# Optimization experiments

Measured on AMD Instinct MI355X. Metric: run time of the kernel, lower is better.

Reference implementation:

```python
import jax, jax.numpy as jnp
import numpy as np
from jax.scipy.special import logsumexp, gammaln

B, F, T = 4, 256, 256
K, L, C, D, N = 8, 1, 10, 156, 2
A00, A10 = 0.99, 0.99
NEG = -1.0e9


def setup_inputs():
    ks = jax.random.split(jax.random.key(0), 12)
    def p(i, shape, s=0.05):
        return jax.random.normal(ks[i], shape, jnp.float32) * s
    A = jnp.array([[A00, 1.0 - A00], [A10, 1.0 - A10]], jnp.float32)
    return dict(
        h=jax.random.normal(ks[0], (B, F, T), jnp.float32),
        logit_lo1=jax.random.normal(ks[1], (K, C, 1), jnp.float32),
        log_A=jnp.broadcast_to(jnp.log(A), (K, C, N, N)),
        dur_conc=p(2, (K, C, N, L), 1.0),
        dur_rate=p(3, (K, C, N, L), 1.0),
        dur_mix=p(4, (K, C, N, L), 1.0),
        w_mix=p(5, (F, F)), b_mix=jnp.zeros((F,), jnp.float32),
        q_attn=p(6, (F,)), w_attn=p(7, (F, F)), b_attn=jnp.zeros((F,), jnp.float32),
        w_k=p(8, (K, F)), b_k=jnp.zeros((K,), jnp.float32),
        bn_gamma=jnp.ones((F,), jnp.float32), bn_beta=jnp.zeros((F,), jnp.float32),
        w_em=p(9, (C * N * K, F)), b_em=jnp.zeros((C * N * K,), jnp.float32),
    )


def gamma_duration(conc_raw, rate_raw, mix_raw):
    # L-component gamma mixture over durations 1..D, normalized over D. [K,C,N,D]
    a = jax.nn.softplus(conc_raw) + 1e-4
    b = jax.nn.softplus(rate_raw) + 1e-4
    d = jnp.arange(1, D + 1, dtype=jnp.float32)
    logpdf = (a[..., None] * jnp.log(b)[..., None] - gammaln(a)[..., None]
              + (a[..., None] - 1.0) * jnp.log(d) - b[..., None] * d)  # [K,C,N,L,D]
    logw = jax.nn.log_softmax(mix_raw, axis=-1)
    lp = logsumexp(logw[..., None] + logpdf, axis=-2)  # [K,C,N,D]
    return jax.nn.log_softmax(lp, axis=-1)


def emission(h, bn_gamma, bn_beta, w_em, b_em):
    # BatchNorm1d (training-mode batch stats) -> ReLU -> 1x1 Conv -> rearrange
    mean = h.mean(axis=(0, 2), keepdims=True)
    var = ((h - mean) ** 2).mean(axis=(0, 2), keepdims=True)
    x = (h - mean) / jnp.sqrt(var + 1e-5) * bn_gamma[None, :, None] + bn_beta[None, :, None]
    x = jax.nn.relu(x)
    y = jnp.einsum('of,bft->bot', w_em, x) + b_em[None, :, None]  # [B, K*C*N, T]
    return y.reshape(B, K, C, N, T)


def mixture_ratio(h, w_mix, b_mix, q_attn, w_attn, b_attn, w_k, b_k):
    # 1x1 Conv -> ReLU -> attention pooling over T -> Linear(F,K) -> log_softmax
    x = jax.nn.relu(jnp.einsum('of,bft->bot', w_mix, h) + b_mix[None, :, None])  # [B,F,T]
    scores = jnp.einsum('f,bft->bt', q_attn, x)
    w = jax.nn.softmax(scores, axis=-1)
    pooled = jnp.einsum('bft,bt->bf', x, w)
    z = pooled @ w_attn.T + b_attn
    logits = z @ w_k.T + b_k
    return jax.nn.log_softmax(logits, axis=-1)  # [B,K]


def compute_log_b(logp_x):
    # log_b[...,d,t] = sum_{i=0}^{d} logp_x[...,t-i] (d<=t), else -10.  [B,K,C,N,D,T]
    src = jnp.arange(T)[None, :] - jnp.arange(D)[:, None]  # [D,T]
    valid = src >= 0
    g = logp_x[:, :, :, :, jnp.clip(src, 0, T - 1)]        # [B,K,C,N,D,T]
    g = jnp.where(valid, g, 0.0)
    lb = jnp.cumsum(g, axis=-2)
    return jnp.where(valid, lb, -10.0)


def hsmm_forward(logp_x, log_lo, logp_d, log_A):
    log_b = compute_log_b(logp_x)                          # [B,K,C,N,D,T]
    log_c = logp_d[None, :, :, :, :, None] + log_b
    darange = jnp.arange(D)
    dclip = jnp.minimum(jnp.arange(T), D - 1)
    lb_diag = log_b[:, :, :, :, dclip, jnp.arange(T)]      # [B,K,C,N,T]
    xs = (jnp.arange(T),
          jnp.moveaxis(log_c, -1, 0),                      # [T,B,K,C,N,D]
          jnp.moveaxis(lb_diag, -1, 0),                    # [T,B,K,C,N]
          jnp.moveaxis(logp_d[:, :, :, dclip], -1, 0))     # [T,K,C,N]
    S0 = jnp.full((B, K, C, N, D), NEG)                    # S[...,j] = s[t-1-j]

    def step(S, x):
        t, logc_t, lbd_t, pd_t = x
        # trans[...,m,j] = lse_n(S[...,n,j] + log_A[n,m])
        trans = logsumexp(S[:, :, :, :, None, :] + log_A[None, :, :, :, :, None], axis=3)
        init_t = log_lo[None] + pd_t[None] + lbd_t         # [B,K,C,N]
        alpha_t = jnp.where(darange == t, init_t[..., None],
                            jnp.where(darange < t, trans + logc_t, NEG))
        s_t = logsumexp(alpha_t, axis=-1)
        S_new = jnp.concatenate([s_t[..., None], S[..., :-1]], axis=-1)
        return S_new, alpha_t

    _, alphas = jax.lax.scan(step, S0, xs)
    return jnp.moveaxis(alphas, 0, -1), log_b              # [B,K,C,N,D,T]


def hsmm_backward(log_b, logp_d, log_A):
    j_idx = jnp.arange(D - 1)
    tau = jnp.arange(T)[None, :] + 1 + j_idx[:, None]      # [D-1,T]
    valid = tau <= T - 1
    # M[...,j,t] = log_b[...,j,t+1+j]
    M = log_b[:, :, :, :, j_idx[:, None], jnp.clip(tau, 0, T - 1)]
    M = jnp.where(valid, M, NEG)
    xs_M = jnp.moveaxis(M[..., :T - 1], -1, 0)             # [T-1,B,K,C,N,D-1]
    pd = logp_d[..., :D - 1]                               # [K,C,N,D-1]
    buf0 = jnp.full((B, K, C, N, D - 1), NEG).at[..., 0].set(0.0)

    def step(buf, M_t):
        val = M_t + buf + pd[None]                         # [B,K,C,m,j]
        tot = log_A[None, :, :, :, :, None] + val[:, :, :, None, :, :]  # [B,K,C,n,m,j]
        beta_t = logsumexp(tot, axis=(4, 5))               # [B,K,C,N]
        buf_new = jnp.concatenate([beta_t[..., None], buf[..., :-1]], axis=-1)
        return buf_new, beta_t

    _, betas = jax.lax.scan(step, buf0, xs_M, reverse=True)
    return jnp.concatenate([jnp.moveaxis(betas, 0, -1),
                            jnp.zeros((B, K, C, N, 1))], axis=-1)  # [B,K,C,N,T]


def calc_logp_event(log_alpha, log_beta, log_pi):
    log_gamma = log_alpha + log_beta[..., None, :]
    Z = logsumexp(log_alpha[..., -1], axis=(-2, -1))       # [B,K,C]
    lp = log_gamma - Z[..., None, None, None]
    return logsumexp(log_pi[:, :, None, None, None, None] + lp, axis=1)  # [B,C,N,D,T]


def calc_p_frame(logp_event):
    d_idx = jnp.arange(D)[:, None]
    s_idx = jnp.arange(T)[None, :]

    def per_t(t):
        mask = (s_idx >= d_idx) & (s_idx >= t) & (s_idx <= t + d_idx)  # [D,T]
        lp = jnp.where(mask[None, None, None], logp_event, NEG)
        return logsumexp(lp, axis=(-2, -1))                # [B,C,N]

    lj = jax.lax.map(per_t, jnp.arange(T))                 # [T,B,C,N]
    pj = jax.nn.softmax(jnp.moveaxis(lj, 0, -1), axis=2)   # [B,C,N,T]
    return pj[:, :, 1]


def reference(h, logit_lo1, log_A, dur_conc, dur_rate, dur_mix, w_mix, b_mix,
              q_attn, w_attn, b_attn, w_k, b_k, bn_gamma, bn_beta, w_em, b_em):
    logp_x = emission(h, bn_gamma, bn_beta, w_em, b_em)    # [B,K,C,N,T]
    log_pi = mixture_ratio(h, w_mix, b_mix, q_attn, w_attn, b_attn, w_k, b_k)
    log_lo = jax.nn.log_sigmoid(jnp.stack([logit_lo1, -logit_lo1], axis=2))[..., 0]  # [K,C,N]
    logp_d = gamma_duration(dur_conc, dur_rate, dur_mix)   # [K,C,N,D]
    log_alpha, log_b = hsmm_forward(logp_x, log_lo, logp_d, log_A)
    log_beta = hsmm_backward(log_b, logp_d, log_A)
    logp_event = calc_logp_event(log_alpha, log_beta, log_pi)
    p_frame = calc_p_frame(logp_event)
    return logp_event, p_frame
```

## Files before the change

### kernel.cpp

```cpp
#include <hip/hip_runtime.h>
#include <math.h>

#define BB_ 4
#define FF_ 256
#define TT_ 256
#define KK_ 8
#define CC_ 10
#define DD_ 156
#define OO_ 160
#define NEGC (-1e9f)

__device__ __forceinline__ float softplusf(float x){
    return fmaxf(x, 0.f) + log1pf(expf(-fabsf(x)));
}
__device__ __forceinline__ float lse2f(float a, float b){
    float m = fmaxf(a, b);
    return m + logf(expf(a-m) + expf(b-m));
}
__device__ __forceinline__ float lse2_fast(float a, float b){
    float m = fmaxf(a, b);
    return m + __logf(__expf(a-m) + __expf(b-m));
}
__device__ __forceinline__ void lse_acc(float &m, float &s, float x){
    if (x > m){ s = s*expf(m-x) + 1.f; m = x; }
    else        s += expf(x-m);
}
__device__ __forceinline__ void lse_acc_fast(float &m, float &s, float x){
    if (x > m){ s = s*__expf(m-x) + 1.f; m = x; }
    else        s += __expf(x-m);
}
__device__ __forceinline__ void wave_lse_reduce(float &m, float &s){
    for (int off = 32; off; off >>= 1){
        float m2 = __shfl_xor(m, off);
        float s2 = __shfl_xor(s, off);
        float M  = fmaxf(m, m2);
        s = s*expf(m-M) + s2*expf(m2-M);
        m = M;
    }
}
template<int CTRL>
__device__ __forceinline__ float dppf(float v){
    return __int_as_float(__builtin_amdgcn_update_dpp(
        0, __float_as_int(v), CTRL, 0xF, 0xF, false));
}
__device__ __forceinline__ float dpp_sum8(float a){
    a = a + dppf<0x122>(a);
    a = a + dppf<0x124>(a);
    a = a + dppf<0x128>(a);
    return a;
}
__device__ __forceinline__ float dpp_max8(float a){
    a = fmaxf(a, dppf<0x122>(a));
    a = fmaxf(a, dppf<0x124>(a));
    a = fmaxf(a, dppf<0x128>(a));
    return a;
}

__global__ void k_bnstats_logpd(const float* __restrict__ h, float* __restrict__ meanv,
                                float* __restrict__ rstdv,
                                const float* __restrict__ conc, const float* __restrict__ rate,
                                const float* __restrict__ logit_lo1, float* __restrict__ logp_d,
                                float* __restrict__ log_lo){
    if (blockIdx.x >= FF_){
        if (threadIdx.x >= 64) return;
        int kcn = blockIdx.x - FF_;
        int lane = threadIdx.x;
        float a  = softplusf(conc[kcn]) + 1e-4f;
        float bb = softplusf(rate[kcn]) + 1e-4f;
        float base = a*logf(bb) - lgammaf(a);
        float vals[3]; int ds[3]; int cnt = 0;
        float m = -1e30f, s = 0.f;
        for (int i = 0; i < 3; ++i){
            int d = lane + i*64;
            if (d < DD_){
                float dv = (float)(d+1);
                float x = base + (a - 1.f)*logf(dv) - bb*dv;
                vals[cnt] = x; ds[cnt] = d; ++cnt;
                lse_acc(m, s, x);
            }
        }
        wave_lse_reduce(m, s);
        float total = m + logf(s);
        for (int i = 0; i < cnt; ++i) logp_d[kcn*DD_ + ds[i]] = vals[i] - total;
        if (lane == 0){
            float x = logit_lo1[kcn >> 1];
            float xx = (kcn & 1) ? -x : x;
            log_lo[kcn] = -softplusf(-xx);
        }
        return;
    }
    int f = blockIdx.x; int tid = threadIdx.x;
    float s = 0.f, s2 = 0.f;
    for (int b = 0; b < BB_; ++b){
        float v = h[(b*FF_ + f)*TT_ + tid];
        s += v; s2 += v*v;
    }
    __shared__ float rs[4], rs2[4];
    for (int off = 32; off; off >>= 1){ s += __shfl_xor(s, off); s2 += __shfl_xor(s2, off); }
    if ((tid & 63) == 0){ rs[tid>>6] = s; rs2[tid>>6] = s2; }
    __syncthreads();
    if (tid == 0){
        float S = rs[0]+rs[1]+rs[2]+rs[3];
        float S2 = rs2[0]+rs2[1]+rs2[2]+rs2[3];
        float mean = S / 1024.f;
        float var = S2 / 1024.f - mean*mean;
        meanv[f] = mean;
        rstdv[f] = rsqrtf(var + 1e-5f);
    }
}

__global__ void k_bnapply(const float* __restrict__ h, const float* __restrict__ meanv,
                          const float* __restrict__ rstdv, const float* __restrict__ gamma,
                          const float* __restrict__ beta, float* __restrict__ xbn){
    int idx = blockIdx.x*256 + threadIdx.x;
    int f = (idx >> 8) & 255;
    float x = (h[idx] - meanv[f]) * rstdv[f] * gamma[f] + beta[f];
    xbn[idx] = fmaxf(x, 0.f);
}

__global__ void k_gemm_em(const float* __restrict__ xbn, const float* __restrict__ w_em,
                          const float* __restrict__ b_em, float* __restrict__ Pout){
    int bid = blockIdx.x;
    int b = bid / OO_, o = bid % OO_;
    int t = threadIdx.x;
    const float* xb = xbn + b*FF_*TT_ + t;
    const float* wr = w_em + o*FF_;
    float acc = b_em[o];
    #pragma unroll 8
    for (int f = 0; f < FF_; ++f) acc += wr[f] * xb[f*TT_];
    __shared__ float buf[256];
    buf[t] = acc; __syncthreads();
    for (int off = 1; off < 256; off <<= 1){
        float x = (t >= off) ? buf[t-off] : 0.f;
        __syncthreads();
        buf[t] += x;
        __syncthreads();
    }
    Pout[bid*TT_ + t] = buf[t];
}

__global__ void k_attnpool(const float* __restrict__ xm, const float* __restrict__ xmT,
                           const float* __restrict__ q,
                           const float* __restrict__ w_attn, const float* __restrict__ b_attn,
                           const float* __restrict__ w_k, const float* __restrict__ b_k,
                           float* __restrict__ log_pi){
    int b = blockIdx.x; int tid = threadIdx.x;
    __shared__ float sc[256], pooled[256], zs[256], red[8];
    const float* xb = xm + b*FF_*TT_;
    float acc = 0.f;
    for (int f = 0; f < FF_; ++f) acc += q[f] * xb[f*TT_ + tid];
    sc[tid] = acc; __syncthreads();
    float v = sc[tid];
    float m = v;
    for (int off = 32; off; off >>= 1) m = fmaxf(m, __shfl_xor(m, off));
    if ((tid & 63) == 0) red[tid>>6] = m;
    __syncthreads();
    m = fmaxf(fmaxf(red[0], red[1]), fmaxf(red[2], red[3]));
    float e = expf(v - m);
    float ssum = e;
    for (int off = 32; off; off >>= 1) ssum += __shfl_xor(ssum, off);
    if ((tid & 63) == 0) red[4 + (tid>>6)] = ssum;
    __syncthreads();
    ssum = red[4]+red[5]+red[6]+red[7];
    __syncthreads();
    sc[tid] = e / ssum; __syncthreads();
    const float* xT = xmT + b*TT_*FF_;
    float pacc = 0.f;
    for (int t2 = 0; t2 < TT_; ++t2) pacc += xT[t2*FF_ + tid] * sc[t2];
    pooled[tid] = pacc; __syncthreads();
    int wv = tid >> 6; int ln = tid & 63;
    for (int ii = 0; ii < 64; ++ii){
        int i = wv*64 + ii;
        float za = 0.f;
        #pragma unroll
        for (int ff = 0; ff < 4; ++ff) za += pooled[ln + 64*ff] * w_attn[i*FF_ + ln + 64*ff];
        for (int off = 32; off; off >>= 1) za += __shfl_xor(za, off);
        if (ln == 0) zs[i] = za + b_attn[i];
    }
    __syncthreads();
    if (wv == 0){
        for (int kk2 = 0; kk2 < KK_; ++kk2){
            float za = 0.f;
            #pragma unroll
            for (int ff = 0; ff < 4; ++ff) za += zs[ln + 64*ff] * w_k[kk2*FF_ + ln + 64*ff];
            for (int off = 32; off; off >>= 1) za += __shfl_xor(za, off);
            if (ln == 0) red[kk2] = za + b_k[kk2];
        }
    }
    __syncthreads();
    if (tid == 0){
        float mm = -1e30f;
        for (int i = 0; i < KK_; ++i) mm = fmaxf(mm, red[i]);
        float su = 0.f;
        for (int i = 0; i < KK_; ++i) su += expf(red[i] - mm);
        sc[0] = mm + logf(su);
    }
    __syncthreads();
    if (tid < KK_) log_pi[b*KK_ + tid] = red[tid] - sc[0];
}

__global__ __launch_bounds__(256) void k_scan_mix(const float* __restrict__ P,
                          const float* __restrict__ logp_d,
                          const float* __restrict__ log_lo, const float* __restrict__ log_A,
                          float* __restrict__ s_hist, float* __restrict__ Zout,
                          float* __restrict__ beta,
                          const float* __restrict__ h, const float* __restrict__ w_mix,
                          const float* __restrict__ b_mix, float* __restrict__ xm,
                          float* __restrict__ xmT){
    __shared__ float L[11056];
    if (blockIdx.x >= 2*BB_*KK_*CC_/4){
        int bid = blockIdx.x - 2*BB_*KK_*CC_/4;
        int b = bid >> 8, o = bid & 255;
        int t = threadIdx.x;
        const float* hb = h + b*FF_*TT_ + t;
        const float* wr = w_mix + o*FF_;
        float acc = b_mix[o];
        #pragma unroll 8
        for (int f = 0; f < FF_; ++f) acc += wr[f] * hb[f*TT_];
        float v = fmaxf(acc, 0.f);
        xm[bid*TT_ + t] = v;
        xmT[(b*TT_ + t)*FF_ + o] = v;
        return;
    }
    if (threadIdx.x >= 64) return;
    int sbid = blockIdx.x;
    float* hist = L;
    float* pdL  = L + 8*424;
    float* EL   = pdL + 8*168;
    float* PL   = EL + 8*204;
    float* oL   = PL + 8*257;
    float* fsL  = oL + 8*257;
    float* ctL  = fsL + 8*36;
    int lane = threadIdx.x;
    int ch = lane >> 4, r = lane & 15, n = r & 1, q = r >> 1;
    int g = ch*2 + n, go = g ^ 1;
    bool fwd = sbid < (BB_*KK_*CC_/4);
    int gid0 = (fwd ? sbid : sbid - BB_*KK_*CC_/4) * 4;
    int dlim = fwd ? DD_ : (DD_-1);
    for (int idx = lane; idx < 8*168; idx += 64){
        int g2 = idx/168, d2 = idx%168;
        int gg = gid0 + (g2>>1); int c3 = gg % CC_, k3 = (gg/CC_) % KK_;
        pdL[g2*168 + d2] = (d2 < dlim) ? logp_d[((k3*CC_+c3)*2+(g2&1))*DD_ + d2] : -1e30f;
    }
    for (int idx = lane; idx < 4*512; idx += 64){
        int c2 = idx >> 9, j = idx & 511;
        PL[(c2*2 + (j>>8))*257 + (j&255)] = P[(size_t)(gid0+c2)*512 + j];
    }
    int gidc = gid0 + ch; int c = gidc % CC_, k = (gidc/CC_) % KK_;
    const float* Akc = log_A + (k*CC_+c)*4;
    float Epdn[4], Epdf[16];
    #pragma unroll
    for (int i = 0; i < 4; ++i)  Epdn[i] = __expf(pdL[g*168 + q + 8*i]);
    #pragma unroll
    for (int i = 0; i < 16; ++i) Epdf[i] = __expf(pdL[g*168 + 32 + q + 8*i]);

    if (fwd){
        for (int idx = lane; idx < 8*160; idx += 64)
            hist[(idx/160)*424 + (idx%160)] = -1e30f;
        float Aself = Akc[3*n], Across = Akc[2-n];
        float EAs = __expf(Aself);
        float EAc = __expf(Across);
        float llo = log_lo[(k*CC_+c)*2 + n];
        float Etp, pre[4];
        for (int t0 = 0; t0 < TT_; t0 += 32){
            asm volatile("" ::: "memory");
            float v[20];
            #pragma unroll
            for (int i = 0; i < 20; ++i) v[i] = hist[g*424 + t0 + q + 8*i];
            float z[10];
            #pragma unroll
            for (int i = 0; i < 10; ++i) z[i] = fmaxf(v[2*i], v[2*i+1]);
            #pragma unroll
            for (int i = 0; i < 5; ++i) z[i] = fmaxf(z[2*i], z[2*i+1]);
            float mt = fmaxf(fmaxf(fmaxf(z[0],z[1]), fmaxf(z[2],z[3])), z[4]);
            mt = dpp_max8(mt);
            float pm = -1e30f;
            #pragma unroll
            for (int j = 0; j < 4; ++j){
                int t = t0 + q + 8*j;
                pm = fmaxf(pm, (t < 168) ? pdL[g*168 + t] : -1e30f);
            }
            pm = dpp_max8(pm);
            mt = fmaxf(mt, llo + pm);
            #pragma unroll
            for (int i = 0; i < 20; ++i) EL[g*204 + q + 8*i] = __expf(v[i] - mt);
            float mto = dppf<0xB1>(mt);
            #pragma unroll
            for (int j = 0; j < 4; ++j){
                int tt = q + 8*j; int t = t0 + tt;
                float dP = PL[go*257 + t] - PL[g*257 + t];
                ctL[g*36 + tt] = fminf(EAc * __expf(dP + mto - mt), 1e15f);
            }
            asm volatile("" ::: "memory");
            for (int tt = 0; tt < 32; ++tt){
                float a0 = 0.f, a1 = 0.f;
                #pragma unroll
                for (int i = 0; i < 16; i += 2){
                    a0 = fmaf(EL[g*204 + 127 + tt - q - 8*i],     Epdf[i],   a0);
                    a1 = fmaf(EL[g*204 + 127 + tt - q - 8*(i+1)], Epdf[i+1], a1);
                }
                float a = dpp_sum8(a0 + a1);
                int t = t0 + tt;
                float pdt = (t < 168) ? pdL[g*168 + t] : -1e30f;
                if (r < 2) fsL[g*36 + tt] = a + __expf(llo + pdt - mt);
            }
            asm volatile("" ::: "memory");
            Etp = EL[g*204 + 159];
            #pragma unroll
            for (int i = 0; i < 4; ++i) pre[i] = EL[g*204 + 159 - q - 8*i];
            for (int tt = 0; tt < 32; ++tt){
                int t = t0 + tt;
                float x0 = ((q == 0) ? Etp : pre[0]) * Epdn[0];
                float ac = fmaf(pre[1], Epdn[1], x0);
                ac = fmaf(pre[2], Epdn[2], ac);
                ac = fmaf(pre[3], Epdn[3], ac);
                #pragma unroll
                for (int i = 0; i < 4; ++i) pre[i] = EL[g*204 + 160 + tt - q - 8*i];
                float S = dpp_sum8(ac) + fsL[g*36 + tt];
                S = fminf(fmaxf(S, 1e-30f), 1e15f);
                float So = dppf<0xB1>(S);
                float Et = fminf(fmaf(So, ctL[g*36 + tt], S*EAs), 1e30f);
                float lS = __logf(S), lE = __logf(Et);
                if (r < 2){
                    EL[g*204 + 160 + tt] = Et;
                    hist[g*424 + 160 + t] = lE + mt;
                    oL[g*257 + t] = lS + mt + PL[g*257 + t];
                }
                Etp = Et;
            }
        }
        asm volatile("" ::: "memory");
        for (int idx = lane; idx < 4*512; idx += 64){
            int c2 = idx >> 9, j = idx & 511;
            s_hist[(size_t)(gid0+c2)*512 + j] = oL[(c2*2 + (j>>8))*257 + (j&255)];
        }
        if (r == 0) Zout[gidc] = lse2f(oL[(ch*2)*257 + 255], oL[(ch*2+1)*257 + 255]);
    } else {
        for (int idx = lane; idx < 8*168; idx += 64)
            hist[(idx/168)*424 + 256 + (idx%168)] = -1e30f;
        if (lane < 8){
            hist[lane*424 + 255] = PL[lane*257 + 255];
            oL[lane*257 + 255] = 0.f;
        }
        float Aown = Akc[3*n], Aoth = Akc[n+1];
        float EAo = __expf(Aown);
        float EAx = __expf(Aoth);
        float Ewp, pre[4];
        for (int t0 = TT_-32; t0 >= 0; t0 -= 32){
            asm volatile("" ::: "memory");
            float v[20];
            #pragma unroll
            for (int i = 0; i < 20; ++i) v[i] = hist[g*424 + t0 + 32 + q + 8*i];
            float z[10];
            #pragma unroll
            for (int i = 0; i < 10; ++i) z[i] = fmaxf(v[2*i], v[2*i+1]);
            #pragma unroll
            for (int i = 0; i < 5; ++i) z[i] = fmaxf(z[2*i], z[2*i+1]);
            float mw = fmaxf(fmaxf(fmaxf(z[0],z[1]), fmaxf(z[2],z[3])), z[4]);
            mw = dpp_max8(mw);
            mw = fmaxf(mw, PL[g*257 + 255]);
            #pragma unroll
            for (int i = 0; i < 20; ++i) EL[g*204 + 32 + q + 8*i] = __expf(v[i] - mw);
            float mwo = dppf<0xB1>(mw);
            #pragma unroll
            for (int j = 0; j < 4; ++j){
                int tt = q + 8*j; int t = t0 + tt;
                float dP = PL[g*257 + t] - PL[go*257 + t];
                ctL[g*36 + tt] = fminf(EAx * __expf(dP + mwo - mw), 1e15f);
            }
            if (t0 == TT_-32 && r < 2)
                EL[g*204 + 31] = __expf(hist[g*424 + 255] - mw);
            asm volatile("" ::: "memory");
            for (int tt = 0; tt < 32; ++tt){
                float a0 = 0.f, a1 = 0.f;
                #pragma unroll
                for (int i = 0; i < 16; i += 2){
                    a0 = fmaf(EL[g*204 + tt + 33 + q + 8*i],     Epdf[i],   a0);
                    a1 = fmaf(EL[g*204 + tt + 33 + q + 8*(i+1)], Epdf[i+1], a1);
                }
                float a = dpp_sum8(a0 + a1);
                if (r < 2) fsL[g*36 + tt] = a;
            }
            asm volatile("" ::: "memory");
            int tts = (t0 == TT_-32) ? 30 : 31;
            Ewp = EL[g*204 + tts + 1];
            #pragma unroll
            for (int i = 0; i < 4; ++i) pre[i] = EL[g*204 + tts + 1 + q + 8*i];
            for (int tt = tts; tt >= 0; --tt){
                int t = t0 + tt;
                float x0 = ((q == 0) ? Ewp : pre[0]) * Epdn[0];
                float ac = fmaf(pre[1], Epdn[1], x0);
                ac = fmaf(pre[2], Epdn[2], ac);
                ac = fmaf(pre[3], Epdn[3], ac);
                #pragma unroll
                for (int i = 0; i < 4; ++i) pre[i] = EL[g*204 + tt + q + 8*i];
                float W = dpp_sum8(ac) + fsL[g*36 + tt];
                W = fminf(fmaxf(W, 1e-30f), 1e15f);
                float Wo = dppf<0xB1>(W);
                float Ewt = fminf(fmaf(Wo, ctL[g*36 + tt], W*EAo), 1e30f);
                float lE = __logf(Ewt);
                if (r < 2){
                    EL[g*204 + tt] = Ewt;
                    float wt = lE + mw;
                    hist[g*424 + t] = wt;
                    oL[g*257 + t] = wt - PL[g*257 + t];
                }
                Ewp = Ewt;
            }
        }
        asm volatile("" ::: "memory");
        for (int idx = lane; idx < 4*512; idx += 64){
            int c2 = idx >> 9, j = idx & 511;
            beta[(size_t)(gid0+c2)*512 + j] = oL[(c2*2 + (j>>8))*257 + (j&255)];
        }
    }
}

__global__ void k_logpevent(const float* __restrict__ P, const float* __restrict__ s_hist,
                            const float* __restrict__ beta, const float* __restrict__ logp_d,
                            const float* __restrict__ log_lo, const float* __restrict__ log_A,
                            const float* __restrict__ log_pi, const float* __restrict__ Zv,
                            float* __restrict__ out){
    int bid = blockIdx.x;
    int d = bid % DD_; int rem = bid / DD_;
    int n = rem & 1; int cc = (rem >> 1) % CC_; int b = rem / (2*CC_);
    int t = threadIdx.x;
    float m = -1e30f, s = 0.f;
    for (int k = 0; k < KK_; ++k){
        const float* Pn  = P + (((b*KK_+k)*CC_+cc)*2 + n)*TT_;
        const float* pdn = logp_d + ((k*CC_+cc)*2 + n)*DD_;
        float alpha;
        if (d > t){
            alpha = NEGC;
        } else if (d == t){
            alpha = log_lo[(k*CC_+cc)*2 + n] + pdn[t] + Pn[t];
        } else {
            const float* sh = s_hist + (((b*KK_+k)*CC_+cc)*2)*TT_;
            float u0 = sh[t-1-d]       + log_A[(k*CC_+cc)*4 + n];
            float u1 = sh[TT_ + t-1-d] + log_A[(k*CC_+cc)*4 + 2 + n];
            float tr = lse2_fast(u0, u1);
            alpha = tr + pdn[d] + (Pn[t] - Pn[t-1-d]);
        }
        float term = log_pi[b*KK_ + k] + alpha
                   + beta[(((b*KK_+k)*CC_+cc)*2 + n)*TT_ + t]
                   - Zv[(b*KK_+k)*CC_ + cc];
        lse_acc_fast(m, s, term);
    }
    out[(size_t)bid*TT_ + t] = m + __logf(s);
}

__global__ __launch_bounds__(256) void k_lj(const float* __restrict__ lp_all,
                                            float* __restrict__ ljpart){
    int blk = blockIdx.x;
    int bcn = blk >> 2; int chunk = blk & 3;
    int d0 = chunk * 39;
    const float* lp = lp_all + (size_t)bcn*DD_*TT_;
    int tid = threadIdx.x;
    int wv = tid >> 6; int ln = tid & 63;
    __shared__ float Rp[39][TT_+1];
    for (int rr = wv; rr < 39; rr += 4){
        const float* row = lp + (d0 + rr)*TT_;
        float carry = 0.f;
        if (ln == 0) Rp[rr][0] = 0.f;
        #pragma unroll
        for (int seg = 0; seg < 4; ++seg){
            float v = __expf(fminf(row[seg*64 + ln], 60.f));
            #pragma unroll
            for (int off = 1; off < 64; off <<= 1){
                float u = __shfl_up(v, off);
                if (ln >= off) v += u;
            }
            v += carry;
            Rp[rr][1 + seg*64 + ln] = v;
            carry = __shfl(v, 63);
        }
    }
    __syncthreads();
    float acc = 0.f;
    int t = tid;
    #pragma unroll 4
    for (int rr = 0; rr < 39; ++rr){
        int d = d0 + rr;
        int lo = max(t, d);
        int hi = min(t + d, TT_-1);
        acc += Rp[rr][hi+1] - Rp[rr][lo];
    }
    ljpart[(bcn*4 + chunk)*TT_ + t] = acc;
}

__global__ void k_pframe(const float* __restrict__ ljpart, float* __restrict__ out2){
    int idx = blockIdx.x*256 + threadIdx.x;
    int t = idx & 255; int bc = idx >> 8;
    const float* p0 = ljpart + (size_t)(bc*2 + 0)*4*TT_;
    const float* p1 = ljpart + (size_t)(bc*2 + 1)*4*TT_;
    float s0 = (p0[t] + p0[TT_+t]) + (p0[2*TT_+t] + p0[3*TT_+t]);
    float s1 = (p1[t] + p1[TT_+t]) + (p1[2*TT_+t] + p1[3*TT_+t]);
    float l0 = __logf(fmaxf(s0, 1e-38f));
    float l1 = __logf(fmaxf(s1, 1e-38f));
    float mm = fmaxf(l0, l1);
    float e0 = __expf(l0 - mm), e1 = __expf(l1 - mm);
    out2[idx] = e1 / (e0 + e1);
}

extern "C" void kernel_launch(void* const* d_in, const int* in_sizes, int n_in,
                              void* d_out, int out_size, void* d_ws, size_t ws_size,
                              hipStream_t stream){
    const float* h         = (const float*)d_in[0];
    const float* logit_lo1 = (const float*)d_in[1];
    const float* log_A     = (const float*)d_in[2];
    const float* dur_conc  = (const float*)d_in[3];
    const float* dur_rate  = (const float*)d_in[4];
    const float* w_mix     = (const float*)d_in[6];
    const float* b_mix     = (const float*)d_in[7];
    const float* q_attn    = (const float*)d_in[8];
    const float* w_attn    = (const float*)d_in[9];
    const float* b_attn    = (const float*)d_in[10];
    const float* w_k       = (const float*)d_in[11];
    const float* b_k       = (const float*)d_in[12];
    const float* bn_gamma  = (const float*)d_in[13];
    const float* bn_beta   = (const float*)d_in[14];
    const float* w_em      = (const float*)d_in[15];
    const float* b_em      = (const float*)d_in[16];

    float* out  = (float*)d_out;
    float* out2 = out + (size_t)BB_*CC_*2*DD_*TT_;

    float* ws = (float*)d_ws;
    float* Pbuf   = ws;                 ws += BB_*OO_*TT_;
    float* s_hist = ws;                 ws += BB_*OO_*TT_;
    float* beta   = ws;                 ws += BB_*OO_*TT_;
    float* xbn    = ws;                 ws += BB_*FF_*TT_;
    float* xm     = ws;                 ws += BB_*FF_*TT_;
    float* xmT    = ws;                 ws += BB_*FF_*TT_;
    float* logp_d = ws;                 ws += KK_*CC_*2*DD_;
    float* log_lo = ws;                 ws += KK_*CC_*2;
    float* log_pi = ws;                 ws += BB_*KK_;
    float* Zv     = ws;                 ws += BB_*KK_*CC_;
    float* meanv  = ws;                 ws += FF_;
    float* rstdv  = ws;                 ws += FF_;
    float* ljpart = ws;                 ws += BB_*CC_*2*4*TT_;

    hipLaunchKernelGGL(k_bnstats_logpd, dim3(FF_ + KK_*CC_*2), dim3(256), 0, stream,
                       h, meanv, rstdv, dur_conc, dur_rate, logit_lo1, logp_d, log_lo);
    hipLaunchKernelGGL(k_bnapply,  dim3(BB_*FF_),       dim3(256), 0, stream, h, meanv, rstdv, bn_gamma, bn_beta, xbn);
    hipLaunchKernelGGL(k_gemm_em,  dim3(BB_*OO_),       dim3(256), 0, stream, xbn, w_em, b_em, Pbuf);
    hipLaunchKernelGGL(k_scan_mix, dim3(2*BB_*KK_*CC_/4 + BB_*FF_), dim3(256), 0, stream,
                       Pbuf, logp_d, log_lo, log_A, s_hist, Zv, beta,
                       h, w_mix, b_mix, xm, xmT);
    hipLaunchKernelGGL(k_attnpool, dim3(BB_),           dim3(256), 0, stream, xm, xmT, q_attn, w_attn, b_attn, w_k, b_k, log_pi);
    hipLaunchKernelGGL(k_logpevent,dim3(BB_*CC_*2*DD_), dim3(256), 0, stream, Pbuf, s_hist, beta, logp_d, log_lo, log_A, log_pi, Zv, out);
    hipLaunchKernelGGL(k_lj,       dim3(BB_*CC_*2*4),   dim3(256), 0, stream, out, ljpart);
    hipLaunchKernelGGL(k_pframe,   dim3(BB_*CC_),       dim3(256), 0, stream, ljpart, out2);
}
```

Measured before the change: 246.0 us.

## Tile emission GEMM in shared memory and stage logp_event inputs per block

The emission GEMM now has each block compute 16 output channels over all T. It stages 32-feature slices of x and the weights in shared memory and does the prefix sum with wavefront shuffles instead of one block per output row. k_logpevent now loads the per-(b,c,n) history, beta, P and duration tables into shared memory once and loops over 39 durations per block, replacing one block per duration. Both are meant to cut redundant global loads, but grid sizes drop to 40 and 320 blocks, which may underfill the GPU's compute units.

```diff
diff --git a/kernel.cpp b/kernel.cpp
--- a/kernel.cpp
+++ b/kernel.cpp
@@ -118,25 +118,64 @@
     xbn[idx] = fmaxf(x, 0.f);
 }
 
-__global__ void k_gemm_em(const float* __restrict__ xbn, const float* __restrict__ w_em,
+__global__ __launch_bounds__(256) void k_gemm_em(const float* __restrict__ xbn,
+                          const float* __restrict__ w_em,
                           const float* __restrict__ b_em, float* __restrict__ Pout){
-    int bid = blockIdx.x;
-    int b = bid / OO_, o = bid % OO_;
-    int t = threadIdx.x;
-    const float* xb = xbn + b*FF_*TT_ + t;
-    const float* wr = w_em + o*FF_;
-    float acc = b_em[o];
-    #pragma unroll 8
-    for (int f = 0; f < FF_; ++f) acc += wr[f] * xb[f*TT_];
-    __shared__ float buf[256];
-    buf[t] = acc; __syncthreads();
-    for (int off = 1; off < 256; off <<= 1){
-        float x = (t >= off) ? buf[t-off] : 0.f;
+    __shared__ float Xs[32][TT_];
+    __shared__ float Wt[32][16];
+    __shared__ float wsum[16][4];
+    int blk = blockIdx.x;
+    int b = blk / 10, o0 = (blk % 10) * 16;
+    int tid = threadIdx.x;
+    int wv = tid >> 6, ln = tid & 63;
+    const float* xsrc = xbn + b*FF_*TT_;
+    float acc[16];
+    #pragma unroll
+    for (int o = 0; o < 16; ++o) acc[o] = 0.f;
+    for (int kc = 0; kc < 8; ++kc){
         __syncthreads();
-        buf[t] += x;
+        for (int idx = tid; idx < 32*256; idx += 256){
+            int f = idx >> 8, t2 = idx & 255;
+            Xs[f][t2] = xsrc[(kc*32 + f)*TT_ + t2];
+        }
+        for (int idx = tid; idx < 32*16; idx += 256){
+            int f = idx >> 4, o = idx & 15;
+            Wt[f][o] = w_em[(o0 + o)*FF_ + kc*32 + f];
+        }
         __syncthreads();
-    }
-    Pout[bid*TT_ + t] = buf[t];
+        #pragma unroll 4
+        for (int f = 0; f < 32; ++f){
+            float xv = Xs[f][tid];
+            float4 w0 = *reinterpret_cast<const float4*>(&Wt[f][0]);
+            float4 w1 = *reinterpret_cast<const float4*>(&Wt[f][4]);
+            float4 w2 = *reinterpret_cast<const float4*>(&Wt[f][8]);
+            float4 w3 = *reinterpret_cast<const float4*>(&Wt[f][12]);
+            acc[0]  = fmaf(w0.x, xv, acc[0]);  acc[1]  = fmaf(w0.y, xv, acc[1]);
+            acc[2]  = fmaf(w0.z, xv, acc[2]);  acc[3]  = fmaf(w0.w, xv, acc[3]);
+            acc[4]  = fmaf(w1.x, xv, acc[4]);  acc[5]  = fmaf(w1.y, xv, acc[5]);
+            acc[6]  = fmaf(w1.z, xv, acc[6]);  acc[7]  = fmaf(w1.w, xv, acc[7]);
+            acc[8]  = fmaf(w2.x, xv, acc[8]);  acc[9]  = fmaf(w2.y, xv, acc[9]);
+            acc[10] = fmaf(w2.z, xv, acc[10]); acc[11] = fmaf(w2.w, xv, acc[11]);
+            acc[12] = fmaf(w3.x, xv, acc[12]); acc[13] = fmaf(w3.y, xv, acc[13]);
+            acc[14] = fmaf(w3.z, xv, acc[14]); acc[15] = fmaf(w3.w, xv, acc[15]);
+        }
+    }
+    __syncthreads();
+    #pragma unroll 1
+    for (int o = 0; o < 16; ++o){
+        float v = acc[o] + b_em[o0 + o];
+        #pragma unroll
+        for (int off = 1; off < 64; off <<= 1){
+            float u = __shfl_up(v, off);
+            if (ln >= off) v += u;
+        }
+        if (ln == 63) wsum[o][wv] = v;
+        __syncthreads();
+        float carry = 0.f;
+        for (int w = 0; w < 4; ++w) if (w < wv) carry += wsum[o][w];
+        v += carry;
+        Pout[(b*OO_ + o0 + o)*TT_ + tid] = v;
+    }
 }
 
 __global__ void k_attnpool(const float* __restrict__ xm, const float* __restrict__ xmT,
@@ -416,37 +455,63 @@
     }
 }
 
-__global__ void k_logpevent(const float* __restrict__ P, const float* __restrict__ s_hist,
+__global__ __launch_bounds__(256) void k_logpevent(const float* __restrict__ P,
+                            const float* __restrict__ s_hist,
                             const float* __restrict__ beta, const float* __restrict__ logp_d,
                             const float* __restrict__ log_lo, const float* __restrict__ log_A,
                             const float* __restrict__ log_pi, const float* __restrict__ Zv,
                             float* __restrict__ out){
-    int bid = blockIdx.x;
-    int d = bid % DD_; int rem = bid / DD_;
+    __shared__ float sh0[KK_][TT_];
+    __shared__ float sh1[KK_][TT_];
+    __shared__ float bet[KK_][TT_];
+    __shared__ float Pns[KK_][TT_];
+    __shared__ float pds[KK_][256];
+    __shared__ float lpz_s[KK_], llo_s[KK_], lA0[KK_], lA1[KK_];
+    int blk = blockIdx.x;
+    int dchunk = blk & 3; int rem = blk >> 2;
     int n = rem & 1; int cc = (rem >> 1) % CC_; int b = rem / (2*CC_);
-    int t = threadIdx.x;
-    float m = -1e30f, s = 0.f;
-    for (int k = 0; k < KK_; ++k){
-        const float* Pn  = P + (((b*KK_+k)*CC_+cc)*2 + n)*TT_;
-        const float* pdn = logp_d + ((k*CC_+cc)*2 + n)*DD_;
-        float alpha;
-        if (d > t){
-            alpha = NEGC;
-        } else if (d == t){
-            alpha = log_lo[(k*CC_+cc)*2 + n] + pdn[t] + Pn[t];
-        } else {
-            const float* sh = s_hist + (((b*KK_+k)*CC_+cc)*2)*TT_;
-            float u0 = sh[t-1-d]       + log_A[(k*CC_+cc)*4 + n];
-            float u1 = sh[TT_ + t-1-d] + log_A[(k*CC_+cc)*4 + 2 + n];
-            float tr = lse2_fast(u0, u1);
-            alpha = tr + pdn[d] + (Pn[t] - Pn[t-1-d]);
-        }
-        float term = log_pi[b*KK_ + k] + alpha
-                   + beta[(((b*KK_+k)*CC_+cc)*2 + n)*TT_ + t]
-                   - Zv[(b*KK_+k)*CC_ + cc];
-        lse_acc_fast(m, s, term);
-    }
-    out[(size_t)bid*TT_ + t] = m + __logf(s);
+    int tid = threadIdx.x;
+    for (int idx = tid; idx < KK_*TT_; idx += 256){
+        int k = idx >> 8, t2 = idx & 255;
+        int base2 = (((b*KK_+k)*CC_+cc)*2);
+        sh0[k][t2] = s_hist[(size_t)base2*TT_ + t2];
+        sh1[k][t2] = s_hist[(size_t)base2*TT_ + TT_ + t2];
+        bet[k][t2] = beta[(size_t)(base2 + n)*TT_ + t2];
+        Pns[k][t2] = P[(base2 + n)*TT_ + t2];
+        int kc = (k*CC_+cc)*2 + n;
+        pds[k][t2] = (t2 < DD_) ? logp_d[kc*DD_ + t2] : -1e30f;
+    }
+    if (tid < KK_){
+        int k = tid;
+        int kc = (k*CC_+cc)*2 + n;
+        lpz_s[k] = log_pi[b*KK_ + k] - Zv[(b*KK_+k)*CC_ + cc];
+        llo_s[k] = log_lo[kc];
+        lA0[k] = log_A[(k*CC_+cc)*4 + n];
+        lA1[k] = log_A[(k*CC_+cc)*4 + 2 + n];
+    }
+    __syncthreads();
+    int t = tid;
+    size_t obase = (size_t)(((b*CC_+cc)*2 + n)*DD_)*TT_;
+    for (int j = 0; j < 39; ++j){
+        int d = dchunk*39 + j;
+        int tau = t - 1 - d; int tauc = tau < 0 ? 0 : tau;
+        float m = -1e30f, s = 0.f;
+        #pragma unroll
+        for (int k = 0; k < KK_; ++k){
+            float alpha;
+            if (d > t){
+                alpha = NEGC;
+            } else if (d == t){
+                alpha = llo_s[k] + pds[k][t] + Pns[k][t];
+            } else {
+                float u0 = sh0[k][tauc] + lA0[k];
+                float u1 = sh1[k][tauc] + lA1[k];
+                alpha = lse2_fast(u0, u1) + pds[k][d] + (Pns[k][t] - Pns[k][tauc]);
+            }
+            lse_acc_fast(m, s, lpz_s[k] + alpha + bet[k][t]);
+        }
+        out[obase + (size_t)d*TT_ + t] = m + __logf(s);
+    }
 }
 
 __global__ __launch_bounds__(256) void k_lj(const float* __restrict__ lp_all,
@@ -543,12 +608,12 @@
     hipLaunchKernelGGL(k_bnstats_logpd, dim3(FF_ + KK_*CC_*2), dim3(256), 0, stream,
                        h, meanv, rstdv, dur_conc, dur_rate, logit_lo1, logp_d, log_lo);
     hipLaunchKernelGGL(k_bnapply,  dim3(BB_*FF_),       dim3(256), 0, stream, h, meanv, rstdv, bn_gamma, bn_beta, xbn);
-    hipLaunchKernelGGL(k_gemm_em,  dim3(BB_*OO_),       dim3(256), 0, stream, xbn, w_em, b_em, Pbuf);
+    hipLaunchKernelGGL(k_gemm_em,  dim3(BB_*10),        dim3(256), 0, stream, xbn, w_em, b_em, Pbuf);
     hipLaunchKernelGGL(k_scan_mix, dim3(2*BB_*KK_*CC_/4 + BB_*FF_), dim3(256), 0, stream,
                        Pbuf, logp_d, log_lo, log_A, s_hist, Zv, beta,
                        h, w_mix, b_mix, xm, xmT);
     hipLaunchKernelGGL(k_attnpool, dim3(BB_),           dim3(256), 0, stream, xm, xmT, q_attn, w_attn, b_attn, w_k, b_k, log_pi);
-    hipLaunchKernelGGL(k_logpevent,dim3(BB_*CC_*2*DD_), dim3(256), 0, stream, Pbuf, s_hist, beta, logp_d, log_lo, log_A, log_pi, Zv, out);
+    hipLaunchKernelGGL(k_logpevent,dim3(BB_*CC_*2*4),   dim3(256), 0, stream, Pbuf, s_hist, beta, logp_d, log_lo, log_A, log_pi, Zv, out);
     hipLaunchKernelGGL(k_lj,       dim3(BB_*CC_*2*4),   dim3(256), 0, stream, out, ljpart);
     hipLaunchKernelGGL(k_pframe,   dim3(BB_*CC_),       dim3(256), 0, stream, ljpart, out2);
 }
```

New measurement: 304.3 us. +23.7%, slower.

## Stage per-(b,c,n) inputs in shared memory and loop over duration chunks

Applied to the files above, without the earlier changes.

k_logpevent goes from one block per (b,c,n,d) to one block per (b,c,n,chunk of 39 durations). Each block stages s_hist, beta, P, logp_d and scalar parameters for all K in shared memory once, then reuses them across 39 durations. This removes repeated global loads. The cost is far fewer blocks (320 instead of 12480), which lowers parallelism on a large GPU, and some shared-memory bank traffic from the shifted-index reads.

```diff
diff --git a/kernel.cpp b/kernel.cpp
--- a/kernel.cpp
+++ b/kernel.cpp
@@ -416,37 +416,63 @@
     }
 }
 
-__global__ void k_logpevent(const float* __restrict__ P, const float* __restrict__ s_hist,
+__global__ __launch_bounds__(256) void k_logpevent(const float* __restrict__ P,
+                            const float* __restrict__ s_hist,
                             const float* __restrict__ beta, const float* __restrict__ logp_d,
                             const float* __restrict__ log_lo, const float* __restrict__ log_A,
                             const float* __restrict__ log_pi, const float* __restrict__ Zv,
                             float* __restrict__ out){
-    int bid = blockIdx.x;
-    int d = bid % DD_; int rem = bid / DD_;
+    __shared__ float sh0[KK_][TT_];
+    __shared__ float sh1[KK_][TT_];
+    __shared__ float bet[KK_][TT_];
+    __shared__ float Pns[KK_][TT_];
+    __shared__ float pds[KK_][256];
+    __shared__ float lpz_s[KK_], llo_s[KK_], lA0[KK_], lA1[KK_];
+    int blk = blockIdx.x;
+    int dchunk = blk & 3; int rem = blk >> 2;
     int n = rem & 1; int cc = (rem >> 1) % CC_; int b = rem / (2*CC_);
-    int t = threadIdx.x;
-    float m = -1e30f, s = 0.f;
-    for (int k = 0; k < KK_; ++k){
-        const float* Pn  = P + (((b*KK_+k)*CC_+cc)*2 + n)*TT_;
-        const float* pdn = logp_d + ((k*CC_+cc)*2 + n)*DD_;
-        float alpha;
-        if (d > t){
-            alpha = NEGC;
-        } else if (d == t){
-            alpha = log_lo[(k*CC_+cc)*2 + n] + pdn[t] + Pn[t];
-        } else {
-            const float* sh = s_hist + (((b*KK_+k)*CC_+cc)*2)*TT_;
-            float u0 = sh[t-1-d]       + log_A[(k*CC_+cc)*4 + n];
-            float u1 = sh[TT_ + t-1-d] + log_A[(k*CC_+cc)*4 + 2 + n];
-            float tr = lse2_fast(u0, u1);
-            alpha = tr + pdn[d] + (Pn[t] - Pn[t-1-d]);
-        }
-        float term = log_pi[b*KK_ + k] + alpha
-                   + beta[(((b*KK_+k)*CC_+cc)*2 + n)*TT_ + t]
-                   - Zv[(b*KK_+k)*CC_ + cc];
-        lse_acc_fast(m, s, term);
-    }
-    out[(size_t)bid*TT_ + t] = m + __logf(s);
+    int tid = threadIdx.x;
+    for (int idx = tid; idx < KK_*TT_; idx += 256){
+        int k = idx >> 8, t2 = idx & 255;
+        int base2 = (((b*KK_+k)*CC_+cc)*2);
+        sh0[k][t2] = s_hist[(size_t)base2*TT_ + t2];
+        sh1[k][t2] = s_hist[(size_t)base2*TT_ + TT_ + t2];
+        bet[k][t2] = beta[(size_t)(base2 + n)*TT_ + t2];
+        Pns[k][t2] = P[(base2 + n)*TT_ + t2];
+        int kc = (k*CC_+cc)*2 + n;
+        pds[k][t2] = (t2 < DD_) ? logp_d[kc*DD_ + t2] : -1e30f;
+    }
+    if (tid < KK_){
+        int k = tid;
+        int kc = (k*CC_+cc)*2 + n;
+        lpz_s[k] = log_pi[b*KK_ + k] - Zv[(b*KK_+k)*CC_ + cc];
+        llo_s[k] = log_lo[kc];
+        lA0[k] = log_A[(k*CC_+cc)*4 + n];
+        lA1[k] = log_A[(k*CC_+cc)*4 + 2 + n];
+    }
+    __syncthreads();
+    int t = tid;
+    size_t obase = (size_t)(((b*CC_+cc)*2 + n)*DD_)*TT_;
+    for (int j = 0; j < 39; ++j){
+        int d = dchunk*39 + j;
+        int tau = t - 1 - d; int tauc = tau < 0 ? 0 : tau;
+        float m = -1e30f, s = 0.f;
+        #pragma unroll
+        for (int k = 0; k < KK_; ++k){
+            float alpha;
+            if (d > t){
+                alpha = NEGC;
+            } else if (d == t){
+                alpha = llo_s[k] + pds[k][t] + Pns[k][t];
+            } else {
+                float u0 = sh0[k][tauc] + lA0[k];
+                float u1 = sh1[k][tauc] + lA1[k];
+                alpha = lse2_fast(u0, u1) + pds[k][d] + (Pns[k][t] - Pns[k][tauc]);
+            }
+            lse_acc_fast(m, s, lpz_s[k] + alpha + bet[k][t]);
+        }
+        out[obase + (size_t)d*TT_ + t] = m + __logf(s);
+    }
 }
 
 __global__ __launch_bounds__(256) void k_lj(const float* __restrict__ lp_all,
@@ -548,7 +574,7 @@
                        Pbuf, logp_d, log_lo, log_A, s_hist, Zv, beta,
                        h, w_mix, b_mix, xm, xmT);
     hipLaunchKernelGGL(k_attnpool, dim3(BB_),           dim3(256), 0, stream, xm, xmT, q_attn, w_attn, b_attn, w_k, b_k, log_pi);
-    hipLaunchKernelGGL(k_logpevent,dim3(BB_*CC_*2*DD_), dim3(256), 0, stream, Pbuf, s_hist, beta, logp_d, log_lo, log_A, log_pi, Zv, out);
+    hipLaunchKernelGGL(k_logpevent,dim3(BB_*CC_*2*4),   dim3(256), 0, stream, Pbuf, s_hist, beta, logp_d, log_lo, log_A, log_pi, Zv, out);
     hipLaunchKernelGGL(k_lj,       dim3(BB_*CC_*2*4),   dim3(256), 0, stream, out, ljpart);
     hipLaunchKernelGGL(k_pframe,   dim3(BB_*CC_),       dim3(256), 0, stream, ljpart, out2);
 }
```

After: 277.7 us. 12.9% more time.

## Fuse BN apply into emission GEMM and precompute transition terms per chain

Applied to the files above, without the earlier changes.

BatchNorm scale/shift and ReLU now happen inside the emission GEMM's inner loop, which removes the k_bnapply kernel and the xbn round-trip through memory. A new small kernel k_trm precomputes, per chain and time step, the log-sum-exp over previous states plus the log_A transition minus the prefix sum P, writing it in place into s_hist. With that, k_logpevent needs one gather plus Pn[t] instead of two s_hist loads, an lse2 and an extra P load for each of its 8 k iterations across roughly 12.5k blocks. The cost is one extra launch and the BN affine being recomputed redundantly in each GEMM block.

```diff
diff --git a/kernel.cpp b/kernel.cpp
--- a/kernel.cpp
+++ b/kernel.cpp
@@ -109,26 +109,28 @@
     }
 }
 
-__global__ void k_bnapply(const float* __restrict__ h, const float* __restrict__ meanv,
+__global__ void k_gemm_em(const float* __restrict__ h, const float* __restrict__ meanv,
                           const float* __restrict__ rstdv, const float* __restrict__ gamma,
-                          const float* __restrict__ beta, float* __restrict__ xbn){
-    int idx = blockIdx.x*256 + threadIdx.x;
-    int f = (idx >> 8) & 255;
-    float x = (h[idx] - meanv[f]) * rstdv[f] * gamma[f] + beta[f];
-    xbn[idx] = fmaxf(x, 0.f);
-}
-
-__global__ void k_gemm_em(const float* __restrict__ xbn, const float* __restrict__ w_em,
+                          const float* __restrict__ betav, const float* __restrict__ w_em,
                           const float* __restrict__ b_em, float* __restrict__ Pout){
     int bid = blockIdx.x;
     int b = bid / OO_, o = bid % OO_;
     int t = threadIdx.x;
-    const float* xb = xbn + b*FF_*TT_ + t;
+    __shared__ float af[256], bf[256], buf[256];
+    {
+        float sc = rstdv[t] * gamma[t];
+        af[t] = sc;
+        bf[t] = betav[t] - meanv[t]*sc;
+    }
+    __syncthreads();
+    const float* hb = h + b*FF_*TT_ + t;
     const float* wr = w_em + o*FF_;
     float acc = b_em[o];
     #pragma unroll 8
-    for (int f = 0; f < FF_; ++f) acc += wr[f] * xb[f*TT_];
-    __shared__ float buf[256];
+    for (int f = 0; f < FF_; ++f){
+        float xv = fmaxf(fmaf(hb[f*TT_], af[f], bf[f]), 0.f);
+        acc = fmaf(wr[f], xv, acc);
+    }
     buf[t] = acc; __syncthreads();
     for (int off = 1; off < 256; off <<= 1){
         float x = (t >= off) ? buf[t-off] : 0.f;
@@ -416,35 +418,47 @@
     }
 }
 
-__global__ void k_logpevent(const float* __restrict__ P, const float* __restrict__ s_hist,
+__global__ void k_trm(float* __restrict__ s_hist, const float* __restrict__ P,
+                      const float* __restrict__ log_A){
+    int chain = blockIdx.x;
+    int t = threadIdx.x;
+    int c = chain % CC_, k = (chain/CC_) % KK_;
+    const float* Akc = log_A + (k*CC_+c)*4;
+    size_t base = (size_t)chain*512;
+    float s0 = s_hist[base + t];
+    float s1 = s_hist[base + 256 + t];
+    float P0 = P[base + t];
+    float P1 = P[base + 256 + t];
+    float trm0 = lse2_fast(s0 + Akc[0], s1 + Akc[2]) - P0;
+    float trm1 = lse2_fast(s0 + Akc[1], s1 + Akc[3]) - P1;
+    s_hist[base + t]       = trm0;
+    s_hist[base + 256 + t] = trm1;
+}
+
+__global__ void k_logpevent(const float* __restrict__ P, const float* __restrict__ trm,
                             const float* __restrict__ beta, const float* __restrict__ logp_d,
-                            const float* __restrict__ log_lo, const float* __restrict__ log_A,
-                            const float* __restrict__ log_pi, const float* __restrict__ Zv,
-                            float* __restrict__ out){
+                            const float* __restrict__ log_lo, const float* __restrict__ log_pi,
+                            const float* __restrict__ Zv, float* __restrict__ out){
     int bid = blockIdx.x;
     int d = bid % DD_; int rem = bid / DD_;
     int n = rem & 1; int cc = (rem >> 1) % CC_; int b = rem / (2*CC_);
     int t = threadIdx.x;
+    int tau = t - 1 - d; int tauc = tau < 0 ? 0 : tau;
     float m = -1e30f, s = 0.f;
     for (int k = 0; k < KK_; ++k){
-        const float* Pn  = P + (((b*KK_+k)*CC_+cc)*2 + n)*TT_;
-        const float* pdn = logp_d + ((k*CC_+cc)*2 + n)*DD_;
+        int gk = ((b*KK_+k)*CC_+cc)*2 + n;
+        int kc = (k*CC_+cc)*2 + n;
+        float lpz = log_pi[b*KK_ + k] - Zv[(b*KK_+k)*CC_ + cc];
+        const float* Pn = P + (size_t)gk*TT_;
         float alpha;
         if (d > t){
             alpha = NEGC;
         } else if (d == t){
-            alpha = log_lo[(k*CC_+cc)*2 + n] + pdn[t] + Pn[t];
+            alpha = log_lo[kc] + logp_d[kc*DD_ + t] + Pn[t];
         } else {
-            const float* sh = s_hist + (((b*KK_+k)*CC_+cc)*2)*TT_;
-            float u0 = sh[t-1-d]       + log_A[(k*CC_+cc)*4 + n];
-            float u1 = sh[TT_ + t-1-d] + log_A[(k*CC_+cc)*4 + 2 + n];
-            float tr = lse2_fast(u0, u1);
-            alpha = tr + pdn[d] + (Pn[t] - Pn[t-1-d]);
-        }
-        float term = log_pi[b*KK_ + k] + alpha
-                   + beta[(((b*KK_+k)*CC_+cc)*2 + n)*TT_ + t]
-                   - Zv[(b*KK_+k)*CC_ + cc];
-        lse_acc_fast(m, s, term);
+            alpha = trm[(size_t)gk*TT_ + tauc] + logp_d[kc*DD_ + d] + Pn[t];
+        }
+        lse_acc_fast(m, s, lpz + alpha + beta[(size_t)gk*TT_ + t]);
     }
     out[(size_t)bid*TT_ + t] = m + __logf(s);
 }
@@ -529,7 +543,6 @@
     float* Pbuf   = ws;                 ws += BB_*OO_*TT_;
     float* s_hist = ws;                 ws += BB_*OO_*TT_;
     float* beta   = ws;                 ws += BB_*OO_*TT_;
-    float* xbn    = ws;                 ws += BB_*FF_*TT_;
     float* xm     = ws;                 ws += BB_*FF_*TT_;
     float* xmT    = ws;                 ws += BB_*FF_*TT_;
     float* logp_d = ws;                 ws += KK_*CC_*2*DD_;
@@ -542,13 +555,14 @@
 
     hipLaunchKernelGGL(k_bnstats_logpd, dim3(FF_ + KK_*CC_*2), dim3(256), 0, stream,
                        h, meanv, rstdv, dur_conc, dur_rate, logit_lo1, logp_d, log_lo);
-    hipLaunchKernelGGL(k_bnapply,  dim3(BB_*FF_),       dim3(256), 0, stream, h, meanv, rstdv, bn_gamma, bn_beta, xbn);
-    hipLaunchKernelGGL(k_gemm_em,  dim3(BB_*OO_),       dim3(256), 0, stream, xbn, w_em, b_em, Pbuf);
+    hipLaunchKernelGGL(k_gemm_em,  dim3(BB_*OO_),       dim3(256), 0, stream,
+                       h, meanv, rstdv, bn_gamma, bn_beta, w_em, b_em, Pbuf);
     hipLaunchKernelGGL(k_scan_mix, dim3(2*BB_*KK_*CC_/4 + BB_*FF_), dim3(256), 0, stream,
                        Pbuf, logp_d, log_lo, log_A, s_hist, Zv, beta,
                        h, w_mix, b_mix, xm, xmT);
+    hipLaunchKernelGGL(k_trm,      dim3(BB_*KK_*CC_),   dim3(256), 0, stream, s_hist, Pbuf, log_A);
     hipLaunchKernelGGL(k_attnpool, dim3(BB_),           dim3(256), 0, stream, xm, xmT, q_attn, w_attn, b_attn, w_k, b_k, log_pi);
-    hipLaunchKernelGGL(k_logpevent,dim3(BB_*CC_*2*DD_), dim3(256), 0, stream, Pbuf, s_hist, beta, logp_d, log_lo, log_A, log_pi, Zv, out);
+    hipLaunchKernelGGL(k_logpevent,dim3(BB_*CC_*2*DD_), dim3(256), 0, stream, Pbuf, s_hist, beta, logp_d, log_lo, log_pi, Zv, out);
     hipLaunchKernelGGL(k_lj,       dim3(BB_*CC_*2*4),   dim3(256), 0, stream, out, ljpart);
     hipLaunchKernelGGL(k_pframe,   dim3(BB_*CC_),       dim3(256), 0, stream, ljpart, out2);
 }
```

After: 236.1 us. 4.0% less time.
